# Performance work log

Hardware: AMD Instinct MI355X
Metric: run time of the kernel (lower is better)

The kernel has to match this reference:

```python
import jax, jax.numpy as jnp
import numpy as np

DIM = 2048        # model hidden size
INTER = 1408      # per-expert intermediate size
E = 16            # n_routed_experts
TOPK = 2          # n_activated_experts
S_INTER = 2816    # shared experts intermediate (n_shared_experts * INTER)
T = 4096          # tokens (batch*seq, module flattens to [-1, dim])
ROUTE_SCALE = 1.0


def setup_inputs() -> dict:
    key = jax.random.key(0)
    ks = jax.random.split(key, 8)
    g = lambda k, shape, scale: (jax.random.normal(k, shape, dtype=jnp.float32) * scale)
    return {
        "x": g(ks[0], (T, DIM), 1.0),
        "gate_w": g(ks[1], (E, DIM), 0.02),
        "w1": g(ks[2], (E, INTER, DIM), 0.02),
        "w2": g(ks[3], (E, DIM, INTER), 0.02),
        "w3": g(ks[4], (E, INTER, DIM), 0.02),
        "sw1": g(ks[5], (S_INTER, DIM), 0.02),
        "sw2": g(ks[6], (DIM, S_INTER), 0.02),
        "sw3": g(ks[7], (S_INTER, DIM), 0.02),
    }


def _moe_forward(x, gate_w, w1, w2, w3, sw1, sw2, sw3):
    t = x.shape[0]
    # ---- gate: softmax scores -> top-k experts per token ----
    scores = jax.nn.softmax(x @ gate_w.T, axis=-1)          # [T, E]
    top_w, top_i = jax.lax.top_k(scores, TOPK)              # [T, K]
    top_w = top_w * ROUTE_SCALE
    # dense combine weights [T, E]: zero for unselected experts
    combine = jnp.zeros((t, E), x.dtype).at[jnp.arange(t)[:, None], top_i].add(top_w)
    # ---- routed experts: gated silu MLP per expert, weighted combine ----
    # loop over the small fixed expert count; tokens with combine==0 contribute 0,
    # matching the original scatter/gather dispatch math exactly.
    y = jnp.zeros_like(x)
    for e in range(E):
        h = jax.nn.silu(x @ w1[e].T) * (x @ w3[e].T)        # [T, INTER]
        y = y + (h @ w2[e].T) * combine[:, e:e + 1]
    # ---- shared experts ----
    z = (jax.nn.silu(x @ sw1.T) * (x @ sw3.T)) @ sw2.T      # [T, DIM]
    return y + z


def reference(x, gate_w, w1, w2, w3, sw1, sw2, sw3):
    return _moe_forward(x, gate_w, w1, w2, w3, sw1, sw2, sw3)
```

## Files before the change

### kernel.cpp

```cpp
#include <hip/hip_runtime.h>
#include <hip/hip_bf16.h>
#include <cstdint>
#include <cstddef>

#define TTOK   4096
#define DIM_   2048
#define INTER_ 1408
#define NEXP   16
#define SINTER_ 2816
#define BM 128
#define BN 128
#define BK 64
#define MAXROWS (TTOK*2 + NEXP*BM)
#define MAXMT   (TTOK*2/BM + NEXP)

#define NT_SH_H  ((TTOK/BM) * (SINTER_/BN))
#define NT_RT_H  (MAXMT * (INTER_/BN))
#define NT_H     (NT_SH_H + NT_RT_H)
#define NT_SH_O  ((TTOK/BM) * (DIM_/BN))
#define NT_RT_O  (MAXMT * (DIM_/BN))
#define NT_O     (NT_SH_O + NT_RT_O)

typedef unsigned short u16;
typedef __attribute__((ext_vector_type(8))) short short8;
typedef __attribute__((ext_vector_type(4))) float f32x4;

#define AS3P(p) ((__attribute__((address_space(3))) void*)(p))
#define AS1P(p) ((const __attribute__((address_space(1))) void*)(p))

__device__ __forceinline__ void gll16(const void* g, void* l) {
    __builtin_amdgcn_global_load_lds(AS1P(g), AS3P(l), 16, 0, 0);
}

__device__ __forceinline__ u16 f2bf(float f) {
    __hip_bfloat16 h = __float2bfloat16(f);
    union { __hip_bfloat16 h; u16 u; } c; c.h = h; return c.u;
}

__device__ __forceinline__ unsigned pk2(float a, float b) {
    unsigned r;
    asm("v_cvt_pk_bf16_f32 %0, %1, %2" : "=v"(r) : "v"(a), "v"(b));
    return r;
}

__device__ __forceinline__ int4 pack8(float4 a, float4 b) {
    int4 r;
    r.x = (int)pk2(a.x, a.y);
    r.y = (int)pk2(a.z, a.w);
    r.z = (int)pk2(b.x, b.y);
    r.w = (int)pk2(b.z, b.w);
    return r;
}

#define NW8  ((long)NEXP * INTER_ * DIM_ / 8)
#define NSW8 ((long)SINTER_ * DIM_ / 8)
#define NX8  ((long)TTOK * DIM_ / 8)
#define TOT8 (3 * NW8 + 3 * NSW8 + NX8)

__global__ void cvt_all_kernel(
    const float* __restrict__ w1, const float* __restrict__ w2,
    const float* __restrict__ w3, const float* __restrict__ sw1,
    const float* __restrict__ sw2, const float* __restrict__ sw3,
    const float* __restrict__ x,
    u16* __restrict__ w1b, u16* __restrict__ w2b, u16* __restrict__ w3b,
    u16* __restrict__ sw1b, u16* __restrict__ sw2b, u16* __restrict__ sw3b,
    u16* __restrict__ xb,
    int* __restrict__ perm_rt, float* __restrict__ pw_rt,
    int* __restrict__ misc, int* __restrict__ zrow,
    float* __restrict__ outz)
{
    const long stride = (long)gridDim.x * 256;
    const long gid = (long)blockIdx.x * 256 + threadIdx.x;

    if (gid < MAXROWS) { perm_rt[gid] = -1; pw_rt[gid] = 0.f; }
    if (gid < 32)      misc[gid] = 0;
    if (gid < 1024)    zrow[gid] = 0;
    for (long i = gid; i < (long)TTOK * DIM_ / 4; i += stride)
        *(float4*)(outz + i * 4) = make_float4(0.f, 0.f, 0.f, 0.f);

    for (long i = gid; i < TOT8; i += stride) {
        const float* s; u16* d; long off;
        if      (i <     NW8)              { s = w1;  d = w1b;  off = i; }
        else if (i < 2 * NW8)              { s = w2;  d = w2b;  off = i - NW8; }
        else if (i < 3 * NW8)              { s = w3;  d = w3b;  off = i - 2 * NW8; }
        else if (i < 3 * NW8 + NSW8)       { s = sw1; d = sw1b; off = i - 3 * NW8; }
        else if (i < 3 * NW8 + 2 * NSW8)   { s = sw2; d = sw2b; off = i - 3 * NW8 - NSW8; }
        else if (i < 3 * NW8 + 3 * NSW8)   { s = sw3; d = sw3b; off = i - 3 * NW8 - 2 * NSW8; }
        else                               { s = x;   d = xb;   off = i - 3 * NW8 - 3 * NSW8; }
        const float4* s4 = (const float4*)(s + off * 8);
        float4 a = s4[0], b = s4[1];
        *(int4*)(d + off * 8) = pack8(a, b);
    }
}

__global__ void gate_kernel(const float* __restrict__ x, const float* __restrict__ gw,
                            int* __restrict__ topi, float* __restrict__ topw,
                            int* __restrict__ misc) {
    int t = blockIdx.x;
    int lane = threadIdx.x;
    const float* xr = x + (size_t)t * DIM_;
    float acc[NEXP];
#pragma unroll
    for (int e = 0; e < NEXP; e++) acc[e] = 0.f;
#pragma unroll
    for (int i = 0; i < 8; i++) {
        int k = i * 256 + lane * 4;
        float4 xv = *(const float4*)(xr + k);
#pragma unroll
        for (int e = 0; e < NEXP; e++) {
            float4 gv = *(const float4*)(gw + (size_t)e * DIM_ + k);
            acc[e] += xv.x * gv.x + xv.y * gv.y + xv.z * gv.z + xv.w * gv.w;
        }
    }
#pragma unroll
    for (int e = 0; e < NEXP; e++) {
        float v = acc[e];
        for (int off = 32; off > 0; off >>= 1) v += __shfl_down(v, off);
        acc[e] = v;
    }
    if (lane == 0) {
        float m = acc[0];
#pragma unroll
        for (int e = 1; e < NEXP; e++) m = fmaxf(m, acc[e]);
        float p[NEXP]; float s = 0.f;
#pragma unroll
        for (int e = 0; e < NEXP; e++) { p[e] = __expf(acc[e] - m); s += p[e]; }
        int i0 = 0; float v0 = p[0];
#pragma unroll
        for (int e = 1; e < NEXP; e++) if (p[e] > v0) { v0 = p[e]; i0 = e; }
        int i1 = -1; float v1 = -1.f;
#pragma unroll
        for (int e = 0; e < NEXP; e++) if (e != i0 && p[e] > v1) { v1 = p[e]; i1 = e; }
        float inv = 1.f / s;
        topi[2 * t] = i0; topi[2 * t + 1] = i1;
        topw[2 * t] = v0 * inv; topw[2 * t + 1] = v1 * inv;
        atomicAdd(&misc[i0], 1);
        atomicAdd(&misc[i1], 1);
    }
}

__global__ void scan_kernel(int* misc) {
    int* counts = misc;
    int* base   = misc + 32;
    int* te     = misc + 48;
    int* tr     = misc + 128;
    int b = 0, tt = 0;
    for (int e = 0; e < NEXP; e++) {
        int c = counts[e];
        int nt = (c + BM - 1) >> 7;
        base[e] = b;
        for (int i = 0; i < nt; i++) { te[tt] = e; tr[tt] = b + i * BM; tt++; }
        b += nt * BM;
    }
    for (int i = tt; i < MAXMT; i++) te[i] = -1;
}

__global__ void scatter_kernel(const int* __restrict__ topi, const float* __restrict__ topw,
                               int* __restrict__ misc, int* __restrict__ perm,
                               float* __restrict__ pw) {
    int t = blockIdx.x * 256 + threadIdx.x;
    if (t >= TTOK) return;
    int* fill = misc + 16;
    int* base = misc + 32;
#pragma unroll
    for (int k = 0; k < 2; k++) {
        int e = topi[2 * t + k];
        int pos = base[e] + atomicAdd(&fill[e], 1);
        perm[pos] = t;
        pw[pos] = topw[2 * t + k];
    }
}


__global__ __launch_bounds__(256, 2) void gemm_h13_m(
    const u16* __restrict__ Xb,
    const u16* __restrict__ W1b, const u16* __restrict__ W3b,
    u16* __restrict__ HS, u16* __restrict__ HR,
    const int* __restrict__ perm,
    const int* __restrict__ te, const int* __restrict__ tr,
    const u16* __restrict__ zrow,
    int K, int chunk)
{
    const int q = (blockIdx.x & 7) * chunk + (blockIdx.x >> 3);
    if (q >= NT_H) return;
    int im, jn, N, slot0; size_t eoff; u16* H; bool gather;
    if (q < NT_SH_H) {
        im = q % (TTOK / BM); jn = q / (TTOK / BM);
        N = SINTER_; slot0 = im * BM; eoff = (size_t)NEXP * INTER_ * DIM_;
        H = HS; gather = false;
    } else {
        int q2 = q - NT_SH_H;
        im = q2 % MAXMT; jn = q2 / MAXMT;
        int e = te[im]; if (e < 0) return;
        slot0 = tr[im]; N = INTER_; eoff = (size_t)e * INTER_ * DIM_;
        H = HR; gather = true;
    }
    const int n0 = jn * BN;
    const u16* W1 = W1b + eoff;
    const u16* W3 = W3b + eoff;

    __shared__ __align__(16) u16 As[BM * BK];
    __shared__ __align__(16) u16 B1s[BM * BK];
    __shared__ __align__(16) u16 B3s[BM * BK];

    const int tid = threadIdx.x;
    const int lane = tid & 63, wid = tid >> 6;
    const int wr = wid >> 1, wc = wid & 1;
    const int col = lane & 15, kg = lane >> 4;

    const int lr8 = lane >> 3;
    const int kb  = ((lane & 7) ^ lr8) * 8;
    const int rB0 = wid * 32 + lr8;
    const u16* gA[4];
#pragma unroll
    for (int i = 0; i < 4; i++) {
        int row = slot0 + rB0 + 8 * i;
        if (gather) {
            int ta = perm[row];
            gA[i] = (ta >= 0 ? Xb + (size_t)ta * K : zrow) + kb;
        } else {
            gA[i] = Xb + (size_t)row * K + kb;
        }
    }
    const u16* g1 = W1 + (size_t)(n0 + rB0) * K + kb;
    const u16* g3 = W3 + (size_t)(n0 + rB0) * K + kb;

    const int ldsI = (wid * 32) * BK;
    const int swr = col & 7;

    f32x4 acc1[4][4] = {};
    f32x4 acc3[4][4] = {};

    for (int k0 = 0; k0 < K; k0 += BK) {
#pragma unroll
        for (int i = 0; i < 4; i++) {
            gll16(gA[i] + k0, As + ldsI + i * 8 * BK);
            gll16(g1 + (size_t)(8 * i) * K + k0, B1s + ldsI + i * 8 * BK);
            gll16(g3 + (size_t)(8 * i) * K + k0, B3s + ldsI + i * 8 * BK);
        }
        __syncthreads();

        short8 a[4][2];
#pragma unroll
        for (int mi = 0; mi < 4; mi++)
#pragma unroll
            for (int t = 0; t < 2; t++) {
                int cc = kg + 4 * t;
                a[mi][t] = *(const short8*)(As + (wr * 64 + mi * 16 + col) * BK + ((cc ^ swr) * 8));
            }
#pragma unroll
        for (int t = 0; t < 2; t++) {
#pragma unroll
            for (int ni = 0; ni < 4; ni++) {
                int cc = kg + 4 * t;
                int off = (wc * 64 + ni * 16 + col) * BK + ((cc ^ swr) * 8);
                short8 v1 = *(const short8*)(B1s + off);
                short8 v3 = *(const short8*)(B3s + off);
#pragma unroll
                for (int mi = 0; mi < 4; mi++) {
                    acc1[mi][ni] = __builtin_amdgcn_mfma_f32_16x16x32_bf16(a[mi][t], v1, acc1[mi][ni], 0, 0, 0);
                    acc3[mi][ni] = __builtin_amdgcn_mfma_f32_16x16x32_bf16(a[mi][t], v3, acc3[mi][ni], 0, 0, 0);
                }
            }
        }
        __syncthreads();
    }

#pragma unroll
    for (int mi = 0; mi < 4; mi++) {
#pragma unroll
        for (int j = 0; j < 4; j++) {
            int row = slot0 + wr * 64 + mi * 16 + kg * 4 + j;
#pragma unroll
            for (int ni = 0; ni < 4; ni++) {
                float v1 = acc1[mi][ni][j];
                float v3 = acc3[mi][ni][j];
                float hv = v1 / (1.f + __expf(-v1)) * v3;
                int c = n0 + wc * 64 + ni * 16 + col;
                H[(size_t)row * N + c] = f2bf(hv);
            }
        }
    }
}


__global__ __launch_bounds__(256, 3) void gemm_out_m(
    const u16* __restrict__ HS, const u16* __restrict__ HR,
    const u16* __restrict__ W2b,
    float* __restrict__ Out,
    const int* __restrict__ perm, const float* __restrict__ pw,
    const int* __restrict__ te, const int* __restrict__ tr,
    int chunk)
{
    const int q = (blockIdx.x & 7) * chunk + (blockIdx.x >> 3);
    if (q >= NT_O) return;
    int im, jn, K, slot0; size_t eoff; const u16* A; bool gather;
    if (q < NT_SH_O) {
        im = q % (TTOK / BM); jn = q / (TTOK / BM);
        K = SINTER_; slot0 = im * BM; eoff = (size_t)NEXP * INTER_ * DIM_;
        A = HS; gather = false;
    } else {
        int q2 = q - NT_SH_O;
        im = q2 % MAXMT; jn = q2 / MAXMT;
        int e = te[im]; if (e < 0) return;
        slot0 = tr[im]; K = INTER_; eoff = (size_t)e * INTER_ * DIM_;
        A = HR; gather = true;
    }
    const int n0 = jn * BN;
    const u16* W2 = W2b + eoff;

    __shared__ __align__(16) u16 As[BM * BK];
    __shared__ __align__(16) u16 Bs[BM * BK];

    const int tid = threadIdx.x;
    const int lane = tid & 63, wid = tid >> 6;
    const int wr = wid >> 1, wc = wid & 1;
    const int col = lane & 15, kg = lane >> 4;

    const int lr8 = lane >> 3;
    const int kb  = ((lane & 7) ^ lr8) * 8;
    const int rB0 = wid * 32 + lr8;
    const u16* gA = A + (size_t)(slot0 + rB0) * K + kb;
    const u16* gB = W2 + (size_t)(n0 + rB0) * K + kb;
    const int ldsI = (wid * 32) * BK;
    const int swr = col & 7;

    f32x4 acc[4][4] = {};

    for (int k0 = 0; k0 < K; k0 += BK) {
#pragma unroll
        for (int i = 0; i < 4; i++) {
            gll16(gA + (size_t)(8 * i) * K + k0, As + ldsI + i * 8 * BK);
            gll16(gB + (size_t)(8 * i) * K + k0, Bs + ldsI + i * 8 * BK);
        }
        __syncthreads();

        short8 a[4][2];
#pragma unroll
        for (int mi = 0; mi < 4; mi++)
#pragma unroll
            for (int t = 0; t < 2; t++) {
                int cc = kg + 4 * t;
                a[mi][t] = *(const short8*)(As + (wr * 64 + mi * 16 + col) * BK + ((cc ^ swr) * 8));
            }
#pragma unroll
        for (int t = 0; t < 2; t++) {
#pragma unroll
            for (int ni = 0; ni < 4; ni++) {
                int cc = kg + 4 * t;
                int off = (wc * 64 + ni * 16 + col) * BK + ((cc ^ swr) * 8);
                short8 bv = *(const short8*)(Bs + off);
#pragma unroll
                for (int mi = 0; mi < 4; mi++)
                    acc[mi][ni] = __builtin_amdgcn_mfma_f32_16x16x32_bf16(a[mi][t], bv, acc[mi][ni], 0, 0, 0);
            }
        }
        __syncthreads();
    }

#pragma unroll
    for (int mi = 0; mi < 4; mi++) {
#pragma unroll
        for (int j = 0; j < 4; j++) {
            int rloc = wr * 64 + mi * 16 + kg * 4 + j;
            int slot = slot0 + rloc;
            int token; float w;
            if (gather) {
                token = perm[slot];
                if (token < 0) continue;
                w = pw[slot];
            } else {
                token = slot;
                w = 1.f;
            }
#pragma unroll
            for (int ni = 0; ni < 4; ni++) {
                int c = n0 + wc * 64 + ni * 16 + col;
                atomicAdd(&Out[(size_t)token * DIM_ + c], acc[mi][ni][j] * w);
            }
        }
    }
}


extern "C" void kernel_launch(void* const* d_in, const int* in_sizes, int n_in,
                              void* d_out, int out_size, void* d_ws, size_t ws_size,
                              hipStream_t stream) {
    (void)in_sizes; (void)n_in; (void)out_size; (void)ws_size;
    const float* x   = (const float*)d_in[0];
    const float* gw  = (const float*)d_in[1];
    const float* w1  = (const float*)d_in[2];
    const float* w2  = (const float*)d_in[3];
    const float* w3  = (const float*)d_in[4];
    const float* sw1 = (const float*)d_in[5];
    const float* sw2 = (const float*)d_in[6];
    const float* sw3 = (const float*)d_in[7];
    float* out = (float*)d_out;

    char* ws = (char*)d_ws;
    size_t off = 0;
    auto take = [&](size_t bytes) -> void* {
        void* p = ws + off;
        off += (bytes + 255) & ~(size_t)255;
        return p;
    };
    u16*   xb      = (u16*)take((size_t)TTOK * DIM_ * 2);
    u16*   hbufS   = (u16*)take((size_t)TTOK * SINTER_ * 2);
    u16*   hbufR   = (u16*)take((size_t)MAXROWS * INTER_ * 2);
    int*   perm_rt = (int*)take((size_t)MAXROWS * 4);
    float* pw_rt   = (float*)take((size_t)MAXROWS * 4);
    int*   topi    = (int*)take((size_t)TTOK * 2 * 4);
    float* topw    = (float*)take((size_t)TTOK * 2 * 4);
    int*   misc    = (int*)take(1024);
    int*   zrow    = (int*)take(4096);
    const size_t nW  = (size_t)NEXP * INTER_ * DIM_;
    const size_t nSW = (size_t)SINTER_ * DIM_;
    u16* w1b  = (u16*)take(nW * 2);
    u16* sw1b = (u16*)take(nSW * 2);
    u16* w3b  = (u16*)take(nW * 2);
    u16* sw3b = (u16*)take(nSW * 2);
    u16* w2b  = (u16*)take(nW * 2);
    u16* sw2b = (u16*)take(nSW * 2);

    cvt_all_kernel<<<4096, 256, 0, stream>>>(w1, w2, w3, sw1, sw2, sw3, x,
                                             w1b, w2b, w3b, sw1b, sw2b, sw3b, xb,
                                             perm_rt, pw_rt, misc, zrow, out);
    gate_kernel<<<TTOK, 64, 0, stream>>>(x, gw, topi, topw, misc);
    scan_kernel<<<1, 1, 0, stream>>>(misc);
    scatter_kernel<<<TTOK / 256, 256, 0, stream>>>(topi, topw, misc, perm_rt, pw_rt);

    gemm_h13_m<<<NT_H, 256, 0, stream>>>(
        xb, w1b, w3b, hbufS, hbufR, perm_rt, misc + 48, misc + 128,
        (const u16*)zrow, DIM_, NT_H / 8);

    gemm_out_m<<<NT_O, 256, 0, stream>>>(
        hbufS, hbufR, w2b, out, perm_rt, pw_rt, misc + 48, misc + 128,
        NT_O / 8);
}
```

Baseline: 818.8 us.

## Triple-buffer 256x128 down-projection GEMM and fold gate into convert kernel

The output GEMM now uses 512-thread blocks with 256x128 tiles and a three-stage LDS ring. Loads for future k-steps are issued through global_load_lds with explicit vmcnt waits, so memory latency overlaps the MFMA work and there are fewer atomic-adding tiles. The gate computation moves into extra blocks of the convert kernel, four tokens per block, which removes a launch. Expert padding changes to 256-row granularity, with separate 128 and 256 tile tables, and misc is zeroed by a memset. This raises LDS use (about 144KB per block) and adds padded rows for experts with small token counts.

```diff
diff --git a/kernel.cpp b/kernel.cpp
--- a/kernel.cpp
+++ b/kernel.cpp
@@ -11,15 +11,24 @@
 #define BM 128
 #define BN 128
 #define BK 64
-#define MAXROWS (TTOK*2 + NEXP*BM)
-#define MAXMT   (TTOK*2/BM + NEXP)
+#define MAXROWS (TTOK*2 + NEXP*256)
+#define MAXMT128 (MAXROWS/128)
+#define MAXMT256 (MAXROWS/256)
 
 #define NT_SH_H  ((TTOK/BM) * (SINTER_/BN))
-#define NT_RT_H  (MAXMT * (INTER_/BN))
+#define NT_RT_H  (MAXMT128 * (INTER_/BN))
 #define NT_H     (NT_SH_H + NT_RT_H)
-#define NT_SH_O  ((TTOK/BM) * (DIM_/BN))
-#define NT_RT_O  (MAXMT * (DIM_/BN))
+
+#define OBM 256
+#define OBN 128
+#define NT_SH_O  ((TTOK/OBM) * (DIM_/OBN))
+#define NT_RT_O  (MAXMT256 * (DIM_/OBN))
 #define NT_O     (NT_SH_O + NT_RT_O)
+
+#define M_TE   48
+#define M_TR   144
+#define M_TE2  240
+#define M_TR2  288
 
 typedef unsigned short u16;
 typedef __attribute__((ext_vector_type(8))) short short8;
@@ -52,107 +61,123 @@
     return r;
 }
 
+#define WB(NLIT) do { \
+    asm volatile("s_waitcnt vmcnt(" #NLIT ")" ::: "memory"); \
+    __builtin_amdgcn_s_barrier(); \
+    asm volatile("" ::: "memory"); \
+} while (0)
+#define LB() do { \
+    asm volatile("s_waitcnt lgkmcnt(0)" ::: "memory"); \
+    __builtin_amdgcn_s_barrier(); \
+    asm volatile("" ::: "memory"); \
+} while (0)
+
 #define NW8  ((long)NEXP * INTER_ * DIM_ / 8)
 #define NSW8 ((long)SINTER_ * DIM_ / 8)
 #define NX8  ((long)TTOK * DIM_ / 8)
 #define TOT8 (3 * NW8 + 3 * NSW8 + NX8)
+#define CVT_BLK 4096
+#define GATE_BLK (TTOK / 4)
 
 __global__ void cvt_all_kernel(
     const float* __restrict__ w1, const float* __restrict__ w2,
     const float* __restrict__ w3, const float* __restrict__ sw1,
     const float* __restrict__ sw2, const float* __restrict__ sw3,
-    const float* __restrict__ x,
+    const float* __restrict__ x, const float* __restrict__ gw,
     u16* __restrict__ w1b, u16* __restrict__ w2b, u16* __restrict__ w3b,
     u16* __restrict__ sw1b, u16* __restrict__ sw2b, u16* __restrict__ sw3b,
     u16* __restrict__ xb,
     int* __restrict__ perm_rt, float* __restrict__ pw_rt,
     int* __restrict__ misc, int* __restrict__ zrow,
-    float* __restrict__ outz)
+    float* __restrict__ outz,
+    int* __restrict__ topi, float* __restrict__ topw)
 {
     const long stride = (long)gridDim.x * 256;
     const long gid = (long)blockIdx.x * 256 + threadIdx.x;
 
     if (gid < MAXROWS) { perm_rt[gid] = -1; pw_rt[gid] = 0.f; }
-    if (gid < 32)      misc[gid] = 0;
     if (gid < 1024)    zrow[gid] = 0;
     for (long i = gid; i < (long)TTOK * DIM_ / 4; i += stride)
         *(float4*)(outz + i * 4) = make_float4(0.f, 0.f, 0.f, 0.f);
 
-    for (long i = gid; i < TOT8; i += stride) {
-        const float* s; u16* d; long off;
-        if      (i <     NW8)              { s = w1;  d = w1b;  off = i; }
-        else if (i < 2 * NW8)              { s = w2;  d = w2b;  off = i - NW8; }
-        else if (i < 3 * NW8)              { s = w3;  d = w3b;  off = i - 2 * NW8; }
-        else if (i < 3 * NW8 + NSW8)       { s = sw1; d = sw1b; off = i - 3 * NW8; }
-        else if (i < 3 * NW8 + 2 * NSW8)   { s = sw2; d = sw2b; off = i - 3 * NW8 - NSW8; }
-        else if (i < 3 * NW8 + 3 * NSW8)   { s = sw3; d = sw3b; off = i - 3 * NW8 - 2 * NSW8; }
-        else                               { s = x;   d = xb;   off = i - 3 * NW8 - 3 * NSW8; }
-        const float4* s4 = (const float4*)(s + off * 8);
-        float4 a = s4[0], b = s4[1];
-        *(int4*)(d + off * 8) = pack8(a, b);
-    }
-}
-
-__global__ void gate_kernel(const float* __restrict__ x, const float* __restrict__ gw,
-                            int* __restrict__ topi, float* __restrict__ topw,
-                            int* __restrict__ misc) {
-    int t = blockIdx.x;
-    int lane = threadIdx.x;
-    const float* xr = x + (size_t)t * DIM_;
-    float acc[NEXP];
-#pragma unroll
-    for (int e = 0; e < NEXP; e++) acc[e] = 0.f;
-#pragma unroll
-    for (int i = 0; i < 8; i++) {
-        int k = i * 256 + lane * 4;
-        float4 xv = *(const float4*)(xr + k);
+    if (blockIdx.x < CVT_BLK) {
+        const long cstride = (long)CVT_BLK * 256;
+        for (long i = gid; i < TOT8; i += cstride) {
+            const float* s; u16* d; long off;
+            if      (i <     NW8)              { s = w1;  d = w1b;  off = i; }
+            else if (i < 2 * NW8)              { s = w2;  d = w2b;  off = i - NW8; }
+            else if (i < 3 * NW8)              { s = w3;  d = w3b;  off = i - 2 * NW8; }
+            else if (i < 3 * NW8 + NSW8)       { s = sw1; d = sw1b; off = i - 3 * NW8; }
+            else if (i < 3 * NW8 + 2 * NSW8)   { s = sw2; d = sw2b; off = i - 3 * NW8 - NSW8; }
+            else if (i < 3 * NW8 + 3 * NSW8)   { s = sw3; d = sw3b; off = i - 3 * NW8 - 2 * NSW8; }
+            else                               { s = x;   d = xb;   off = i - 3 * NW8 - 3 * NSW8; }
+            const float4* s4 = (const float4*)(s + off * 8);
+            float4 a = s4[0], b = s4[1];
+            *(int4*)(d + off * 8) = pack8(a, b);
+        }
+    } else {
+        int t = (blockIdx.x - CVT_BLK) * 4 + (threadIdx.x >> 6);
+        int lane = threadIdx.x & 63;
+        const float* xr = x + (size_t)t * DIM_;
+        float acc[NEXP];
+#pragma unroll
+        for (int e = 0; e < NEXP; e++) acc[e] = 0.f;
+#pragma unroll
+        for (int i = 0; i < 8; i++) {
+            int k = i * 256 + lane * 4;
+            float4 xv = *(const float4*)(xr + k);
+#pragma unroll
+            for (int e = 0; e < NEXP; e++) {
+                float4 gv = *(const float4*)(gw + (size_t)e * DIM_ + k);
+                acc[e] += xv.x * gv.x + xv.y * gv.y + xv.z * gv.z + xv.w * gv.w;
+            }
+        }
 #pragma unroll
         for (int e = 0; e < NEXP; e++) {
-            float4 gv = *(const float4*)(gw + (size_t)e * DIM_ + k);
-            acc[e] += xv.x * gv.x + xv.y * gv.y + xv.z * gv.z + xv.w * gv.w;
-        }
-    }
-#pragma unroll
-    for (int e = 0; e < NEXP; e++) {
-        float v = acc[e];
-        for (int off = 32; off > 0; off >>= 1) v += __shfl_down(v, off);
-        acc[e] = v;
-    }
-    if (lane == 0) {
-        float m = acc[0];
-#pragma unroll
-        for (int e = 1; e < NEXP; e++) m = fmaxf(m, acc[e]);
-        float p[NEXP]; float s = 0.f;
-#pragma unroll
-        for (int e = 0; e < NEXP; e++) { p[e] = __expf(acc[e] - m); s += p[e]; }
-        int i0 = 0; float v0 = p[0];
-#pragma unroll
-        for (int e = 1; e < NEXP; e++) if (p[e] > v0) { v0 = p[e]; i0 = e; }
-        int i1 = -1; float v1 = -1.f;
-#pragma unroll
-        for (int e = 0; e < NEXP; e++) if (e != i0 && p[e] > v1) { v1 = p[e]; i1 = e; }
-        float inv = 1.f / s;
-        topi[2 * t] = i0; topi[2 * t + 1] = i1;
-        topw[2 * t] = v0 * inv; topw[2 * t + 1] = v1 * inv;
-        atomicAdd(&misc[i0], 1);
-        atomicAdd(&misc[i1], 1);
+            float v = acc[e];
+            for (int off = 32; off > 0; off >>= 1) v += __shfl_down(v, off);
+            acc[e] = v;
+        }
+        if (lane == 0) {
+            float m = acc[0];
+#pragma unroll
+            for (int e = 1; e < NEXP; e++) m = fmaxf(m, acc[e]);
+            float p[NEXP]; float s = 0.f;
+#pragma unroll
+            for (int e = 0; e < NEXP; e++) { p[e] = __expf(acc[e] - m); s += p[e]; }
+            int i0 = 0; float v0 = p[0];
+#pragma unroll
+            for (int e = 1; e < NEXP; e++) if (p[e] > v0) { v0 = p[e]; i0 = e; }
+            int i1 = -1; float v1 = -1.f;
+#pragma unroll
+            for (int e = 0; e < NEXP; e++) if (e != i0 && p[e] > v1) { v1 = p[e]; i1 = e; }
+            float inv = 1.f / s;
+            topi[2 * t] = i0; topi[2 * t + 1] = i1;
+            topw[2 * t] = v0 * inv; topw[2 * t + 1] = v1 * inv;
+            atomicAdd(&misc[i0], 1);
+            atomicAdd(&misc[i1], 1);
+        }
     }
 }
 
 __global__ void scan_kernel(int* misc) {
     int* counts = misc;
     int* base   = misc + 32;
-    int* te     = misc + 48;
-    int* tr     = misc + 128;
-    int b = 0, tt = 0;
+    int* te  = misc + M_TE;
+    int* tr  = misc + M_TR;
+    int* te2 = misc + M_TE2;
+    int* tr2 = misc + M_TR2;
+    int b = 0, tt = 0, tt2 = 0;
     for (int e = 0; e < NEXP; e++) {
         int c = counts[e];
-        int nt = (c + BM - 1) >> 7;
+        int nt2 = (c + 255) >> 8;
         base[e] = b;
-        for (int i = 0; i < nt; i++) { te[tt] = e; tr[tt] = b + i * BM; tt++; }
-        b += nt * BM;
-    }
-    for (int i = tt; i < MAXMT; i++) te[i] = -1;
+        for (int i = 0; i < nt2; i++)     { te2[tt2] = e; tr2[tt2] = b + i * 256; tt2++; }
+        for (int i = 0; i < 2 * nt2; i++) { te[tt]   = e; tr[tt]   = b + i * 128; tt++; }
+        b += nt2 * 256;
+    }
+    for (int i = tt;  i < MAXMT128; i++) te[i]  = -1;
+    for (int i = tt2; i < MAXMT256; i++) te2[i] = -1;
 }
 
 __global__ void scatter_kernel(const int* __restrict__ topi, const float* __restrict__ topw,
@@ -190,7 +215,7 @@
         H = HS; gather = false;
     } else {
         int q2 = q - NT_SH_H;
-        im = q2 % MAXMT; jn = q2 / MAXMT;
+        im = q2 % MAXMT128; jn = q2 / MAXMT128;
         int e = te[im]; if (e < 0) return;
         slot0 = tr[im]; N = INTER_; eoff = (size_t)e * INTER_ * DIM_;
         H = HR; gather = true;
@@ -284,86 +309,105 @@
 }
 
 
-__global__ __launch_bounds__(256, 3) void gemm_out_m(
+__global__ __launch_bounds__(512, 2) void gemm_out_p(
     const u16* __restrict__ HS, const u16* __restrict__ HR,
     const u16* __restrict__ W2b,
     float* __restrict__ Out,
     const int* __restrict__ perm, const float* __restrict__ pw,
-    const int* __restrict__ te, const int* __restrict__ tr,
+    const int* __restrict__ te2, const int* __restrict__ tr2,
     int chunk)
 {
     const int q = (blockIdx.x & 7) * chunk + (blockIdx.x >> 3);
     if (q >= NT_O) return;
     int im, jn, K, slot0; size_t eoff; const u16* A; bool gather;
     if (q < NT_SH_O) {
-        im = q % (TTOK / BM); jn = q / (TTOK / BM);
-        K = SINTER_; slot0 = im * BM; eoff = (size_t)NEXP * INTER_ * DIM_;
+        im = q % (TTOK / OBM); jn = q / (TTOK / OBM);
+        K = SINTER_; slot0 = im * OBM; eoff = (size_t)NEXP * INTER_ * DIM_;
         A = HS; gather = false;
     } else {
         int q2 = q - NT_SH_O;
-        im = q2 % MAXMT; jn = q2 / MAXMT;
-        int e = te[im]; if (e < 0) return;
-        slot0 = tr[im]; K = INTER_; eoff = (size_t)e * INTER_ * DIM_;
+        im = q2 % MAXMT256; jn = q2 / MAXMT256;
+        int e = te2[im]; if (e < 0) return;
+        slot0 = tr2[im]; K = INTER_; eoff = (size_t)e * INTER_ * DIM_;
         A = HR; gather = true;
     }
-    const int n0 = jn * BN;
+    const int n0 = jn * OBN;
     const u16* W2 = W2b + eoff;
 
-    __shared__ __align__(16) u16 As[BM * BK];
-    __shared__ __align__(16) u16 Bs[BM * BK];
+    __shared__ __align__(16) u16 As3[3 * OBM * BK];
+    __shared__ __align__(16) u16 Bs3[3 * OBN * BK];
 
     const int tid = threadIdx.x;
     const int lane = tid & 63, wid = tid >> 6;
-    const int wr = wid >> 1, wc = wid & 1;
+    const int wr = wid >> 2, wcn = wid & 3;
     const int col = lane & 15, kg = lane >> 4;
 
     const int lr8 = lane >> 3;
     const int kb  = ((lane & 7) ^ lr8) * 8;
-    const int rB0 = wid * 32 + lr8;
-    const u16* gA = A + (size_t)(slot0 + rB0) * K + kb;
-    const u16* gB = W2 + (size_t)(n0 + rB0) * K + kb;
-    const int ldsI = (wid * 32) * BK;
+    const u16* gA = A + (size_t)(slot0 + wid * 32 + lr8) * K + kb;
+    const u16* gB = W2 + (size_t)(n0 + wid * 16 + lr8) * K + kb;
+    const int ldsA = (wid * 32) * BK;
+    const int ldsB = (wid * 16) * BK;
     const int swr = col & 7;
 
-    f32x4 acc[4][4] = {};
-
-    for (int k0 = 0; k0 < K; k0 += BK) {
-#pragma unroll
-        for (int i = 0; i < 4; i++) {
-            gll16(gA + (size_t)(8 * i) * K + k0, As + ldsI + i * 8 * BK);
-            gll16(gB + (size_t)(8 * i) * K + k0, Bs + ldsI + i * 8 * BK);
-        }
-        __syncthreads();
-
-        short8 a[4][2];
-#pragma unroll
-        for (int mi = 0; mi < 4; mi++)
-#pragma unroll
-            for (int t = 0; t < 2; t++) {
-                int cc = kg + 4 * t;
-                a[mi][t] = *(const short8*)(As + (wr * 64 + mi * 16 + col) * BK + ((cc ^ swr) * 8));
-            }
-#pragma unroll
-        for (int t = 0; t < 2; t++) {
-#pragma unroll
-            for (int ni = 0; ni < 4; ni++) {
-                int cc = kg + 4 * t;
-                int off = (wc * 64 + ni * 16 + col) * BK + ((cc ^ swr) * 8);
-                short8 bv = *(const short8*)(Bs + off);
-#pragma unroll
-                for (int mi = 0; mi < 4; mi++)
-                    acc[mi][ni] = __builtin_amdgcn_mfma_f32_16x16x32_bf16(a[mi][t], bv, acc[mi][ni], 0, 0, 0);
-            }
-        }
-        __syncthreads();
-    }
-
-#pragma unroll
-    for (int mi = 0; mi < 4; mi++) {
+    f32x4 acc[8][2] = {};
+
+    auto ISSUE = [&](int t) {
+        const int ab = (t % 3) * OBM * BK;
+        const int bb = (t % 3) * OBN * BK;
+        const int ko = t * BK;
+#pragma unroll
+        for (int i = 0; i < 4; i++)
+            gll16(gA + (size_t)(8 * i) * K + ko, As3 + ab + ldsA + i * 8 * BK);
+#pragma unroll
+        for (int i = 0; i < 2; i++)
+            gll16(gB + (size_t)(8 * i) * K + ko, Bs3 + bb + ldsB + i * 8 * BK);
+    };
+
+    const int nt = K / BK;
+    ISSUE(0); ISSUE(1); ISSUE(2);
+
+    for (int t = 0; t < nt; ++t) {
+        if (t + 2 < nt)      WB(12);
+        else if (t + 1 < nt) WB(6);
+        else                 WB(0);
+
+        const u16* Ac = As3 + (t % 3) * OBM * BK;
+        const u16* Bc = Bs3 + (t % 3) * OBN * BK;
+
+        short8 a[8][2], b[2][2];
+#pragma unroll
+        for (int mi = 0; mi < 8; mi++)
+#pragma unroll
+            for (int kk = 0; kk < 2; kk++) {
+                int cc = kg + 4 * kk;
+                a[mi][kk] = *(const short8*)(Ac + (wr * 128 + mi * 16 + col) * BK + ((cc ^ swr) * 8));
+            }
+#pragma unroll
+        for (int ni = 0; ni < 2; ni++)
+#pragma unroll
+            for (int kk = 0; kk < 2; kk++) {
+                int cc = kg + 4 * kk;
+                b[ni][kk] = *(const short8*)(Bc + (wcn * 32 + ni * 16 + col) * BK + ((cc ^ swr) * 8));
+            }
+
+        LB();
+        if (t + 3 < nt) ISSUE(t + 3);
+
+#pragma unroll
+        for (int kk = 0; kk < 2; kk++)
+#pragma unroll
+            for (int ni = 0; ni < 2; ni++)
+#pragma unroll
+                for (int mi = 0; mi < 8; mi++)
+                    acc[mi][ni] = __builtin_amdgcn_mfma_f32_16x16x32_bf16(a[mi][kk], b[ni][kk], acc[mi][ni], 0, 0, 0);
+    }
+
+#pragma unroll
+    for (int mi = 0; mi < 8; mi++) {
 #pragma unroll
         for (int j = 0; j < 4; j++) {
-            int rloc = wr * 64 + mi * 16 + kg * 4 + j;
-            int slot = slot0 + rloc;
+            int slot = slot0 + wr * 128 + mi * 16 + kg * 4 + j;
             int token; float w;
             if (gather) {
                 token = perm[slot];
@@ -374,8 +418,8 @@
                 w = 1.f;
             }
 #pragma unroll
-            for (int ni = 0; ni < 4; ni++) {
-                int c = n0 + wc * 64 + ni * 16 + col;
+            for (int ni = 0; ni < 2; ni++) {
+                int c = n0 + wcn * 32 + ni * 16 + col;
                 atomicAdd(&Out[(size_t)token * DIM_ + c], acc[mi][ni][j] * w);
             }
         }
@@ -411,7 +455,7 @@
     float* pw_rt   = (float*)take((size_t)MAXROWS * 4);
     int*   topi    = (int*)take((size_t)TTOK * 2 * 4);
     float* topw    = (float*)take((size_t)TTOK * 2 * 4);
-    int*   misc    = (int*)take(1024);
+    int*   misc    = (int*)take(2048);
     int*   zrow    = (int*)take(4096);
     const size_t nW  = (size_t)NEXP * INTER_ * DIM_;
     const size_t nSW = (size_t)SINTER_ * DIM_;
@@ -422,18 +466,20 @@
     u16* w2b  = (u16*)take(nW * 2);
     u16* sw2b = (u16*)take(nSW * 2);
 
-    cvt_all_kernel<<<4096, 256, 0, stream>>>(w1, w2, w3, sw1, sw2, sw3, x,
-                                             w1b, w2b, w3b, sw1b, sw2b, sw3b, xb,
-                                             perm_rt, pw_rt, misc, zrow, out);
-    gate_kernel<<<TTOK, 64, 0, stream>>>(x, gw, topi, topw, misc);
+    hipMemsetAsync(misc, 0, 128, stream);
+
+    cvt_all_kernel<<<CVT_BLK + GATE_BLK, 256, 0, stream>>>(
+        w1, w2, w3, sw1, sw2, sw3, x, gw,
+        w1b, w2b, w3b, sw1b, sw2b, sw3b, xb,
+        perm_rt, pw_rt, misc, zrow, out, topi, topw);
     scan_kernel<<<1, 1, 0, stream>>>(misc);
     scatter_kernel<<<TTOK / 256, 256, 0, stream>>>(topi, topw, misc, perm_rt, pw_rt);
 
     gemm_h13_m<<<NT_H, 256, 0, stream>>>(
-        xb, w1b, w3b, hbufS, hbufR, perm_rt, misc + 48, misc + 128,
+        xb, w1b, w3b, hbufS, hbufR, perm_rt, misc + M_TE, misc + M_TR,
         (const u16*)zrow, DIM_, NT_H / 8);
 
-    gemm_out_m<<<NT_O, 256, 0, stream>>>(
-        hbufS, hbufR, w2b, out, perm_rt, pw_rt, misc + 48, misc + 128,
+    gemm_out_p<<<NT_O, 512, 0, stream>>>(
+        hbufS, hbufR, w2b, out, perm_rt, pw_rt, misc + M_TE2, misc + M_TR2,
         NT_O / 8);
 }
```

New measurement: 884.4 us. 8.0% more time.
